# Kernel optimization log

Measured on AMD Instinct MI355X. Metric: run time of the kernel, lower is better.

Reference implementation:

```python
import jax, jax.numpy as jnp
import numpy as np
from jax import lax

TWN_THRESHOLD_FACTOR = 0.05
BN_EPS = 1e-5


@jax.custom_vjp
def _ternary_quant(w, t):
    return (w > t).astype(w.dtype) - (w < -t).astype(w.dtype)

def _tq_fwd(w, t):
    mask = (w > t) | (w < -t)
    return _ternary_quant(w, t), mask

def _tq_bwd(mask, g):
    return (g * mask.astype(g.dtype), jnp.zeros((), g.dtype))

_ternary_quant.defvjp(_tq_fwd, _tq_bwd)


def quantize(w):
    # threshold is detached in the original (weight.detach().abs().max())
    t = TWN_THRESHOLD_FACTOR * jnp.max(jnp.abs(lax.stop_gradient(w)))
    return _ternary_quant(w, t)


def conv2d(x, w, b):
    # x: [N,C,H,W], w: [O,I,K,K], valid conv, stride 1
    y = lax.conv_general_dilated(x, w, (1, 1), 'VALID',
                                 dimension_numbers=('NCHW', 'OIHW', 'NCHW'))
    return y + b[None, :, None, None]


def maxpool2(x):
    return lax.reduce_window(x, -jnp.inf, lax.max,
                             (1, 1, 2, 2), (1, 1, 2, 2), 'VALID')


def bn2d(x, g, b):
    # training-mode batch norm over (N,H,W), biased variance
    m = jnp.mean(x, (0, 2, 3), keepdims=True)
    v = jnp.mean(jnp.square(x - m), (0, 2, 3), keepdims=True)
    return (x - m) * lax.rsqrt(v + BN_EPS) * g[None, :, None, None] + b[None, :, None, None]


def bn1d(x, g, b):
    m = jnp.mean(x, 0, keepdims=True)
    v = jnp.mean(jnp.square(x - m), 0, keepdims=True)
    return (x - m) * lax.rsqrt(v + BN_EPS) * g[None, :] + b[None, :]


def setup_inputs() -> dict:
    key = jax.random.key(0)
    ks = jax.random.split(key, 12)
    N = 4096
    inp = {
        'x': jax.random.normal(ks[0], (N, 1, 28, 28), jnp.float32),
        'w1': jax.random.normal(ks[1], (32, 1, 5, 5), jnp.float32) * 0.2,
        'b1': jnp.zeros((32,), jnp.float32),
        'g1': jnp.ones((32,), jnp.float32),
        'be1': jnp.zeros((32,), jnp.float32),
        'w2': jax.random.normal(ks[2], (64, 32, 5, 5), jnp.float32) * 0.05,
        'b2': jnp.zeros((64,), jnp.float32),
        'g2': jnp.ones((64,), jnp.float32),
        'be2': jnp.zeros((64,), jnp.float32),
        'wf1': jax.random.normal(ks[3], (512, 1024), jnp.float32) * 0.03,
        'bf1': jnp.zeros((512,), jnp.float32),
        'g3': jnp.ones((512,), jnp.float32),
        'be3': jnp.zeros((512,), jnp.float32),
        'wf2': jax.random.normal(ks[4], (10, 512), jnp.float32) * 0.04,
        'bf2': jnp.zeros((10,), jnp.float32),
    }
    return inp


def reference(x, w1, b1, g1, be1, w2, b2, g2, be2, wf1, bf1, g3, be3, wf2, bf2):
    h = jax.nn.relu(bn2d(conv2d(x, quantize(w1), b1), g1, be1))     # [N,32,24,24]
    h = maxpool2(h)                                                  # [N,32,12,12]
    h = jax.nn.relu(bn2d(conv2d(h, quantize(w2), b2), g2, be2))     # [N,64,8,8]
    h = maxpool2(h)                                                  # [N,64,4,4]
    h = h.reshape(h.shape[0], -1)                                    # [N,1024]
    h = jax.nn.relu(bn1d(h @ quantize(wf1).T + bf1, g3, be3))       # [N,512]
    return h @ quantize(wf2).T + bf2                                 # [N,10]
```

## Files before the change

kernel.cpp:

```cpp
#include <hip/hip_runtime.h>

#define TID ((int)threadIdx.x)
typedef unsigned short u16;
typedef short short8 __attribute__((ext_vector_type(8)));
typedef float f32x4 __attribute__((ext_vector_type(4)));

__device__ __forceinline__ u16 f2b(float f) {
    unsigned int x = __float_as_uint(f);
    return (u16)((x + 0x7fffu + ((x >> 16) & 1u)) >> 16);
}
__device__ __forceinline__ float b2f(u16 u) {
    return __uint_as_float(((unsigned int)u) << 16);
}

static constexpr size_t OFF_QW1   = 0;
static constexpr size_t OFF_QWF2  = 3200;
static constexpr size_t OFF_TMAX  = 23680;
static constexpr size_t OFF_SUM1C = 23808;
static constexpr size_t OFF_SSQ1C = 24832;
static constexpr size_t OFF_SUM2  = 25856, OFF_SSQ2 = 26112;
static constexpr size_t OFF_SUM3  = 26368, OFF_SSQ3 = 28416;
static constexpr size_t STATS_BEG = 23680, STATS_END = 30464;
static constexpr size_t OFF_QW2C  = 30720;
static constexpr size_t OFF_QWF1C = 133120;
static constexpr size_t OFF_Y1P   = 1181696;
static constexpr size_t OFF_Y2C   = 38930432;
static constexpr size_t OFF_H2C   = 72484864;
static constexpr size_t OFF_Y3    = 80873472;

__global__ __launch_bounds__(256) void absmax_k(const float* w1, const float* w2,
                                                const float* wf1, const float* wf2,
                                                unsigned int* tmaxbits) {
    int bid = blockIdx.x;
    int b, lb, nb; const float* src; long n;
    if (bid < 1)        { b = 0; src = w1;  n = 800;    lb = bid;       nb = 1;   }
    else if (bid < 9)   { b = 1; src = w2;  n = 51200;  lb = bid - 1;   nb = 8;   }
    else if (bid < 265) { b = 2; src = wf1; n = 524288; lb = bid - 9;   nb = 256; }
    else                { b = 3; src = wf2; n = 5120;   lb = bid - 265; nb = 1;   }
    float m = 0.f;
    for (long i = (long)lb * 256 + TID; i < n; i += (long)nb * 256)
        m = fmaxf(m, fabsf(src[i]));
    __shared__ float red[256];
    red[TID] = m; __syncthreads();
    for (int s = 128; s > 0; s >>= 1) {
        if (TID < s) red[TID] = fmaxf(red[TID], red[TID + s]);
        __syncthreads();
    }
    if (TID == 0) atomicMax(&tmaxbits[b], __float_as_uint(red[0]));
}

__global__ __launch_bounds__(256) void quant_all_k(const float* w1, const float* w2,
                                                   const float* wf1, const float* wf2,
                                                   float* qw1, u16* qw2c, u16* qwf1c,
                                                   float* qwf2, const unsigned int* tmax) {
    int bid = blockIdx.x;
    if (bid < 4) {
        int i = bid * 256 + TID; if (i >= 800) return;
        float t = 0.05f * __uint_as_float(tmax[0]);
        float v = w1[i];
        qw1[i] = (v > t) ? 1.f : ((v < -t) ? -1.f : 0.f);
    } else if (bid < 204) {
        int i = (bid - 4) * 256 + TID;
        float t = 0.05f * __uint_as_float(tmax[1]);
        int ic = i & 31, oc = (i >> 5) & 63, sh = i >> 11;
        float v = w2[(oc * 32 + ic) * 25 + sh];
        qw2c[i] = f2b((v > t) ? 1.f : ((v < -t) ? -1.f : 0.f));
    } else if (bid < 2252) {
        int i = (bid - 204) * 256 + TID;
        float t = 0.05f * __uint_as_float(tmax[2]);
        float v = wf1[i];
        qwf1c[i] = f2b((v > t) ? 1.f : ((v < -t) ? -1.f : 0.f));
    } else {
        int i = (bid - 2252) * 256 + TID;
        float t = 0.05f * __uint_as_float(tmax[3]);
        float v = wf2[i];
        qwf2[i] = (v > t) ? 1.f : ((v < -t) ? -1.f : 0.f);
    }
}

__global__ __launch_bounds__(256) void conv1_fused_k(const float* __restrict__ x,
                                                     const float* __restrict__ qw1,
                                                     u16* __restrict__ y1p,
                                                     float* sum1c, float* ssq1c) {
    __shared__ float wl[800];
    __shared__ float red[4][64];
    for (int i = TID; i < 800; i += 256) wl[i] = qw1[i];
    __syncthreads();
    int p = blockIdx.x * 256 + TID;
    int cg = p & 15, half = (p >> 4) & 1;
    int pr = p >> 5;
    int py = pr % 12, n = pr / 12;
    int l = TID & 63, wv = TID >> 6;
    const float* xb = x + n * 784 + (2 * py) * 28 + half * 12;
    float patch[6][16];
    #pragma unroll
    for (int r = 0; r < 6; r++) {
        const float4* rp = reinterpret_cast<const float4*>(xb + r * 28);
        #pragma unroll
        for (int qq = 0; qq < 4; qq++) {
            float4 v = rp[qq];
            patch[r][qq * 4 + 0] = v.x; patch[r][qq * 4 + 1] = v.y;
            patch[r][qq * 4 + 2] = v.z; patch[r][qq * 4 + 3] = v.w;
        }
    }
    int c0 = cg * 2;
    float st[4];
    float pm[2][6];
    #pragma unroll
    for (int cc = 0; cc < 2; cc++) {
        const float* wr = &wl[(c0 + cc) * 25];
        float a0[12] = {}, a1[12] = {};
        #pragma unroll
        for (int ky = 0; ky < 5; ky++)
            #pragma unroll
            for (int kx = 0; kx < 5; kx++) {
                float w = wr[ky * 5 + kx];
                #pragma unroll
                for (int ox = 0; ox < 12; ox++) {
                    a0[ox] = fmaf(patch[ky][ox + kx], w, a0[ox]);
                    a1[ox] = fmaf(patch[ky + 1][ox + kx], w, a1[ox]);
                }
            }
        float s = 0.f, q = 0.f;
        #pragma unroll
        for (int ox = 0; ox < 12; ox++) {
            s += a0[ox] + a1[ox];
            q = fmaf(a0[ox], a0[ox], q); q = fmaf(a1[ox], a1[ox], q);
        }
        st[cc] = s; st[2 + cc] = q;
        #pragma unroll
        for (int j = 0; j < 6; j++)
            pm[cc][j] = fmaxf(fmaxf(a0[2 * j], a0[2 * j + 1]),
                              fmaxf(a1[2 * j], a1[2 * j + 1]));
    }
    u16* base = y1p + (size_t)n * 4608 + (py * 12 + half * 6) * 32 + c0;
    #pragma unroll
    for (int j = 0; j < 6; j++) {
        unsigned int u = (unsigned int)f2b(pm[0][j]) | ((unsigned int)f2b(pm[1][j]) << 16);
        *reinterpret_cast<unsigned int*>(base + j * 32) = u;
    }
    #pragma unroll
    for (int t = 0; t < 4; t++) {
        st[t] += __shfl_xor(st[t], 16);
        st[t] += __shfl_xor(st[t], 32);
    }
    if (l < 16) {
        #pragma unroll
        for (int t = 0; t < 4; t++) red[wv][l * 4 + t] = st[t];
    }
    __syncthreads();
    if (TID < 64) {
        float v = red[0][TID] + red[1][TID] + red[2][TID] + red[3][TID];
        int t = TID & 3, ch = (TID >> 2) * 2 + (t & 1);
        float* dst = (t < 2 ? sum1c : ssq1c) + (blockIdx.x & 7) * 32 + ch;
        atomicAdd(dst, v);
    }
}

__global__ __launch_bounds__(256) void conv2_k(const u16* __restrict__ y1p,
                                               const u16* __restrict__ qw2c,
                                               u16* __restrict__ y2c,
                                               const float* sum1c, const float* ssq1c,
                                               const float* g1, const float* be1,
                                               float* sum, float* ssq) {
    __shared__ float4 hsm4[1176];
    __shared__ float scs[32], shs[32];
    char* hsraw = (char*)hsm4;
    int n0 = blockIdx.x * 8;
    int l = TID & 63, wv = TID >> 6;
    int oc0 = wv * 16;
    int lm = l & 15, lr = (l >> 3) & 1, ox = l & 7, bq = l >> 4;
    if (TID < 32) {
        float s = 0.f, q = 0.f;
        #pragma unroll
        for (int r = 0; r < 8; r++) { s += sum1c[r * 32 + TID]; q += ssq1c[r * 32 + TID]; }
        float m = s * (1.f / 2359296.f);
        float v = q * (1.f / 2359296.f) - m * m;
        float sc = g1[TID] / sqrtf(v + 1e-5f);
        scs[TID] = sc; shs[TID] = be1[TID] - m * sc;
    }
    __syncthreads();
    float scR[8], shR[8];
    {
        int b = TID & 3;
        #pragma unroll
        for (int j = 0; j < 8; j++) { scR[j] = scs[b * 8 + j]; shR[j] = shs[b * 8 + j]; }
    }
    short8 bw[25];
    #pragma unroll
    for (int sh = 0; sh < 25; sh++)
        bw[sh] = *reinterpret_cast<const short8*>(qw2c + ((size_t)sh * 64 + oc0 + lm) * 32 + bq * 8);
    int xy[5];
    #pragma unroll
    for (int kx = 0; kx < 5; kx++) {
        int xx = ox + kx;
        xy[kx] = lr * 784 + xx * 64 + (((bq + (xx >> 1)) & 3) * 16);
    }
    float sacc = 0.f, s2acc = 0.f;
    {
        const uint4* src = reinterpret_cast<const uint4*>(y1p + (size_t)n0 * 4608);
        #pragma unroll
        for (int k = 0; k < 3; k++) {
            if (k < 2 || TID < 64) {
                int i = TID + k * 256;
                int pix = i >> 2, b = i & 3;
                int y = pix / 12, xx = pix - y * 12;
                union { uint4 v; u16 u[8]; } in, out;
                in.v = src[i];
                #pragma unroll
                for (int j = 0; j < 8; j++)
                    out.u[j] = f2b(fmaxf(fmaf(b2f(in.u[j]), scR[j], shR[j]), 0.f));
                *reinterpret_cast<uint4*>(hsraw + y * 784 + xx * 64 + (((b + (xx >> 1)) & 3) * 16)) = out.v;
            }
        }
    }
    #pragma unroll 1
    for (int s = 0; s < 8; s++) {
        __syncthreads();
        if (s < 7) {
            const uint4* src = reinterpret_cast<const uint4*>(y1p + (size_t)(n0 + s + 1) * 4608);
            char* dst = hsraw + ((s + 1) & 1) * 9408;
            #pragma unroll
            for (int k = 0; k < 3; k++) {
                if (k < 2 || TID < 64) {
                    int i = TID + k * 256;
                    int pix = i >> 2, b = i & 3;
                    int y = pix / 12, xx = pix - y * 12;
                    union { uint4 v; u16 u[8]; } in, out;
                    in.v = src[i];
                    #pragma unroll
                    for (int j = 0; j < 8; j++)
                        out.u[j] = f2b(fmaxf(fmaf(b2f(in.u[j]), scR[j], shR[j]), 0.f));
                    *reinterpret_cast<uint4*>(dst + y * 784 + xx * 64 + (((b + (xx >> 1)) & 3) * 16)) = out.v;
                }
            }
        }
        const char* hb = hsraw + (s & 1) * 9408;
        f32x4 acc[4] = {{0.f,0.f,0.f,0.f},{0.f,0.f,0.f,0.f},{0.f,0.f,0.f,0.f},{0.f,0.f,0.f,0.f}};
        #pragma unroll
        for (int R = 0; R <= 10; R++) {
            short8 a[5];
            #pragma unroll
            for (int kx = 0; kx < 5; kx++)
                a[kx] = *reinterpret_cast<const short8*>(hb + xy[kx] + R * 784);
            #pragma unroll
            for (int mt = 0; mt < 4; mt++) {
                int ky = R - 2 * mt;
                if (ky < 0 || ky > 4) continue;
                #pragma unroll
                for (int kx = 0; kx < 5; kx++)
                    acc[mt] = __builtin_amdgcn_mfma_f32_16x16x32_bf16(a[kx], bw[ky * 5 + kx], acc[mt], 0, 0, 0);
            }
        }
        int n = n0 + s;
        #pragma unroll
        for (int mt = 0; mt < 4; mt++) {
            float v0 = acc[mt][0], v1 = acc[mt][1], v2 = acc[mt][2], v3 = acc[mt][3];
            sacc += v0 + v1 + v2 + v3;
            s2acc += v0 * v0 + v1 * v1 + v2 * v2 + v3 * v3;
            ushort4 u = make_ushort4(f2b(v0), f2b(v1), f2b(v2), f2b(v3));
            *reinterpret_cast<ushort4*>(y2c + (size_t)n * 4096 + (oc0 + lm) * 64 + mt * 16 + bq * 4) = u;
        }
    }
    sacc  += __shfl_xor(sacc, 16);  sacc  += __shfl_xor(sacc, 32);
    s2acc += __shfl_xor(s2acc, 16); s2acc += __shfl_xor(s2acc, 32);
    if (l < 16) { atomicAdd(&sum[oc0 + l], sacc); atomicAdd(&ssq[oc0 + l], s2acc); }
}

__global__ __launch_bounds__(256) void pool2_k(const u16* __restrict__ y2c,
                                               const float* sum2, const float* ssq2,
                                               const float* g2, const float* be2,
                                               u16* __restrict__ h2c) {
    int i = blockIdx.x * 256 + TID;
    int px = i & 3, py = (i >> 2) & 3, oc = (i >> 4) & 63, n = i >> 10;
    float m = sum2[oc] * (1.f / 262144.f);
    float v = ssq2[oc] * (1.f / 262144.f) - m * m;
    float s = g2[oc] / sqrtf(v + 1e-5f);
    float t = be2[oc] - m * s;
    size_t base = (size_t)n * 4096 + oc * 64 + (2 * py) * 8 + 2 * px;
    float a = b2f(y2c[base])     * s + t;
    float b = b2f(y2c[base + 1]) * s + t;
    float c = b2f(y2c[base + 8]) * s + t;
    float d = b2f(y2c[base + 9]) * s + t;
    float mm = fmaxf(fmaxf(fmaxf(fmaxf(0.f, a), b), c), d);
    h2c[i] = f2b(mm);
}

__global__ __launch_bounds__(256) void fc1_k(const u16* __restrict__ h2c,
                                             const u16* __restrict__ qwf1c,
                                             float* __restrict__ y3T,
                                             float* sum3, float* ssq3) {
    __shared__ float4 Asm[576], Bsm[576];
    u16* AsU = (u16*)Asm; u16* BsU = (u16*)Bsm;
    int m0 = blockIdx.x * 64, j0 = blockIdx.y * 64;
    int l = TID & 63, wv = TID >> 6;
    int lm = l & 15, q = l >> 4;
    int r0 = TID >> 3, c0 = TID & 7;
    f32x4 acc[4] = {{0.f,0.f,0.f,0.f},{0.f,0.f,0.f,0.f},{0.f,0.f,0.f,0.f},{0.f,0.f,0.f,0.f}};
    #pragma unroll 1
    for (int kc = 0; kc < 16; kc++) {
        int kk = kc * 64;
        if (kc) __syncthreads();
        #pragma unroll
        for (int i = 0; i < 2; i++) {
            int r = i * 32 + r0;
            *reinterpret_cast<float4*>(AsU + r * 72 + c0 * 8) =
                *reinterpret_cast<const float4*>(h2c + (size_t)(m0 + r) * 1024 + kk + c0 * 8);
            *reinterpret_cast<float4*>(BsU + r * 72 + c0 * 8) =
                *reinterpret_cast<const float4*>(qwf1c + (size_t)(j0 + r) * 1024 + kk + c0 * 8);
        }
        __syncthreads();
        #pragma unroll
        for (int half = 0; half < 2; half++) {
            short8 b = *reinterpret_cast<const short8*>(BsU + (wv * 16 + lm) * 72 + half * 32 + q * 8);
            #pragma unroll
            for (int mt = 0; mt < 4; mt++) {
                short8 a = *reinterpret_cast<const short8*>(AsU + (mt * 16 + lm) * 72 + half * 32 + q * 8);
                acc[mt] = __builtin_amdgcn_mfma_f32_16x16x32_bf16(a, b, acc[mt], 0, 0, 0);
            }
        }
    }
    float s = 0.f, s2 = 0.f;
    #pragma unroll
    for (int mt = 0; mt < 4; mt++) {
        *reinterpret_cast<f32x4*>(y3T + (size_t)(j0 + wv * 16 + lm) * 4096 + m0 + mt * 16 + q * 4) = acc[mt];
        #pragma unroll
        for (int i = 0; i < 4; i++) { float v = acc[mt][i]; s += v; s2 = fmaf(v, v, s2); }
    }
    s  += __shfl_xor(s, 16);  s  += __shfl_xor(s, 32);
    s2 += __shfl_xor(s2, 16); s2 += __shfl_xor(s2, 32);
    if (l < 16) {
        atomicAdd(&sum3[j0 + wv * 16 + l], s);
        atomicAdd(&ssq3[j0 + wv * 16 + l], s2);
    }
}

__global__ __launch_bounds__(256) void fc2_k(const float* __restrict__ y3T,
                                             const float* sum3, const float* ssq3,
                                             const float* g3, const float* be3,
                                             const float* __restrict__ qwf2,
                                             const float* bf2, float* __restrict__ out) {
    __shared__ float wlds[5120];
    __shared__ float part[15][160];
    __shared__ float sc3s[512], sh3s[512];
    for (int i = TID; i < 5120; i += 256) wlds[i] = qwf2[i];
    for (int k = TID; k < 512; k += 256) {
        float m = sum3[k] * (1.f / 4096.f);
        float v = ssq3[k] * (1.f / 4096.f) - m * m;
        float s = g3[k] / sqrtf(v + 1e-5f);
        sc3s[k] = s; sh3s[k] = be3[k] - m * s;
    }
    __syncthreads();
    int nl = TID & 15, ks = TID >> 4;
    int n = blockIdx.x * 16 + nl;
    float acc[10] = {};
    for (int k = ks * 32; k < ks * 32 + 32; k++) {
        float v = fmaxf(y3T[(size_t)k * 4096 + n] * sc3s[k] + sh3s[k], 0.f);
        #pragma unroll
        for (int o = 0; o < 10; o++) acc[o] = fmaf(v, wlds[o * 512 + k], acc[o]);
    }
    if (ks > 0) {
        #pragma unroll
        for (int o = 0; o < 10; o++) part[ks - 1][o * 16 + nl] = acc[o];
    }
    __syncthreads();
    if (ks == 0) {
        #pragma unroll
        for (int o = 0; o < 10; o++) {
            float r = acc[o] + bf2[o];
            #pragma unroll
            for (int j = 0; j < 15; j++) r += part[j][o * 16 + nl];
            out[n * 10 + o] = r;
        }
    }
}

extern "C" void kernel_launch(void* const* d_in, const int* in_sizes, int n_in,
                              void* d_out, int out_size, void* d_ws, size_t ws_size,
                              hipStream_t stream) {
    char* wsb = (char*)d_ws;
    const float* x   = (const float*)d_in[0];
    const float* w1  = (const float*)d_in[1];
    const float* g1  = (const float*)d_in[3];
    const float* be1 = (const float*)d_in[4];
    const float* w2  = (const float*)d_in[5];
    const float* g2  = (const float*)d_in[7];
    const float* be2 = (const float*)d_in[8];
    const float* wf1 = (const float*)d_in[9];
    const float* g3  = (const float*)d_in[11];
    const float* be3 = (const float*)d_in[12];
    const float* wf2 = (const float*)d_in[13];
    const float* bf2 = (const float*)d_in[14];
    float* out = (float*)d_out;

    unsigned int* tmax = (unsigned int*)(wsb + OFF_TMAX);
    float* qw1   = (float*)(wsb + OFF_QW1);
    float* qwf2  = (float*)(wsb + OFF_QWF2);
    u16*   qw2c  = (u16*)(wsb + OFF_QW2C);
    u16*   qwf1c = (u16*)(wsb + OFF_QWF1C);
    u16*   y1p   = (u16*)(wsb + OFF_Y1P);
    u16*   y2c   = (u16*)(wsb + OFF_Y2C);
    u16*   h2c   = (u16*)(wsb + OFF_H2C);
    float* y3    = (float*)(wsb + OFF_Y3);

    float* sum1c = (float*)(wsb + OFF_SUM1C); float* ssq1c = (float*)(wsb + OFF_SSQ1C);
    float* sum2  = (float*)(wsb + OFF_SUM2);  float* ssq2  = (float*)(wsb + OFF_SSQ2);
    float* sum3  = (float*)(wsb + OFF_SUM3);  float* ssq3  = (float*)(wsb + OFF_SSQ3);

    hipMemsetAsync(wsb + STATS_BEG, 0, STATS_END - STATS_BEG, stream);

    absmax_k<<<266, 256, 0, stream>>>(w1, w2, wf1, wf2, tmax);
    quant_all_k<<<2272, 256, 0, stream>>>(w1, w2, wf1, wf2, qw1, qw2c, qwf1c, qwf2, tmax);

    conv1_fused_k<<<6144, 256, 0, stream>>>(x, qw1, y1p, sum1c, ssq1c);
    conv2_k<<<512, 256, 0, stream>>>(y1p, qw2c, y2c, sum1c, ssq1c, g1, be1, sum2, ssq2);
    pool2_k<<<16384, 256, 0, stream>>>(y2c, sum2, ssq2, g2, be2, h2c);
    fc1_k<<<dim3(64, 8), 256, 0, stream>>>(h2c, qwf1c, y3, sum3, ssq3);
    fc2_k<<<256, 256, 0, stream>>>(y3, sum3, ssq3, g3, be3, qwf2, bf2, out);
}
```

Baseline: 235.0 us.

## Enlarge fc1 GEMM tiles with register-prefetch pipelining and vectorize pool loads

The fc1 GEMM moves from 64x64 tiles to 128x128 tiles, with each wave computing a 64x64 sub-tile as 4x4 MFMAs. It uses a 32-wide K step and prefetches the next K slice into registers while the current one is computed, which raises operand reuse per LDS read and hides global load latency. pool2 now reads pairs of adjacent bf16 values as one 32-bit load. The trade-off is a smaller grid (128 blocks on a chip with many CUs), which lowers occupancy and parallelism, and higher register pressure from the 16 accumulators.

```diff
diff --git a/kernel.cpp b/kernel.cpp
--- a/kernel.cpp
+++ b/kernel.cpp
@@ -278,10 +278,10 @@
     float s = g2[oc] / sqrtf(v + 1e-5f);
     float t = be2[oc] - m * s;
     size_t base = (size_t)n * 4096 + oc * 64 + (2 * py) * 8 + 2 * px;
-    float a = b2f(y2c[base])     * s + t;
-    float b = b2f(y2c[base + 1]) * s + t;
-    float c = b2f(y2c[base + 8]) * s + t;
-    float d = b2f(y2c[base + 9]) * s + t;
+    unsigned int u0 = *reinterpret_cast<const unsigned int*>(y2c + base);
+    unsigned int u1 = *reinterpret_cast<const unsigned int*>(y2c + base + 8);
+    float a = b2f((u16)u0) * s + t, b = b2f((u16)(u0 >> 16)) * s + t;
+    float c = b2f((u16)u1) * s + t, d = b2f((u16)(u1 >> 16)) * s + t;
     float mm = fmaxf(fmaxf(fmaxf(fmaxf(0.f, a), b), c), d);
     h2c[i] = f2b(mm);
 }
@@ -290,48 +290,68 @@
                                              const u16* __restrict__ qwf1c,
                                              float* __restrict__ y3T,
                                              float* sum3, float* ssq3) {
-    __shared__ float4 Asm[576], Bsm[576];
-    u16* AsU = (u16*)Asm; u16* BsU = (u16*)Bsm;
-    int m0 = blockIdx.x * 64, j0 = blockIdx.y * 64;
+    __shared__ __align__(16) u16 AsU[128 * 40];
+    __shared__ __align__(16) u16 BsU[128 * 40];
+    int m0 = blockIdx.x * 128, j0 = blockIdx.y * 128;
     int l = TID & 63, wv = TID >> 6;
     int lm = l & 15, q = l >> 4;
-    int r0 = TID >> 3, c0 = TID & 7;
-    f32x4 acc[4] = {{0.f,0.f,0.f,0.f},{0.f,0.f,0.f,0.f},{0.f,0.f,0.f,0.f},{0.f,0.f,0.f,0.f}};
+    int mw = (wv & 1) * 64, jw = (wv >> 1) * 64;
+    f32x4 acc[4][4] = {};
+    float4 pa[2], pb[2];
+    #pragma unroll
+    for (int i = 0; i < 2; i++) {
+        int e = TID + i * 256, m = e >> 2, s = e & 3;
+        pa[i] = *reinterpret_cast<const float4*>(h2c + (size_t)(m0 + m) * 1024 + s * 8);
+        pb[i] = *reinterpret_cast<const float4*>(qwf1c + (size_t)(j0 + m) * 1024 + s * 8);
+    }
     #pragma unroll 1
-    for (int kc = 0; kc < 16; kc++) {
-        int kk = kc * 64;
+    for (int kc = 0; kc < 32; kc++) {
         if (kc) __syncthreads();
         #pragma unroll
         for (int i = 0; i < 2; i++) {
-            int r = i * 32 + r0;
-            *reinterpret_cast<float4*>(AsU + r * 72 + c0 * 8) =
-                *reinterpret_cast<const float4*>(h2c + (size_t)(m0 + r) * 1024 + kk + c0 * 8);
-            *reinterpret_cast<float4*>(BsU + r * 72 + c0 * 8) =
-                *reinterpret_cast<const float4*>(qwf1c + (size_t)(j0 + r) * 1024 + kk + c0 * 8);
+            int e = TID + i * 256, m = e >> 2, s = e & 3;
+            *reinterpret_cast<float4*>(AsU + m * 40 + s * 8) = pa[i];
+            *reinterpret_cast<float4*>(BsU + m * 40 + s * 8) = pb[i];
         }
         __syncthreads();
-        #pragma unroll
-        for (int half = 0; half < 2; half++) {
-            short8 b = *reinterpret_cast<const short8*>(BsU + (wv * 16 + lm) * 72 + half * 32 + q * 8);
-            #pragma unroll
-            for (int mt = 0; mt < 4; mt++) {
-                short8 a = *reinterpret_cast<const short8*>(AsU + (mt * 16 + lm) * 72 + half * 32 + q * 8);
-                acc[mt] = __builtin_amdgcn_mfma_f32_16x16x32_bf16(a, b, acc[mt], 0, 0, 0);
+        if (kc < 31) {
+            int kk = (kc + 1) * 32;
+            #pragma unroll
+            for (int i = 0; i < 2; i++) {
+                int e = TID + i * 256, m = e >> 2, s = e & 3;
+                pa[i] = *reinterpret_cast<const float4*>(h2c + (size_t)(m0 + m) * 1024 + kk + s * 8);
+                pb[i] = *reinterpret_cast<const float4*>(qwf1c + (size_t)(j0 + m) * 1024 + kk + s * 8);
             }
         }
-    }
-    float s = 0.f, s2 = 0.f;
-    #pragma unroll
-    for (int mt = 0; mt < 4; mt++) {
-        *reinterpret_cast<f32x4*>(y3T + (size_t)(j0 + wv * 16 + lm) * 4096 + m0 + mt * 16 + q * 4) = acc[mt];
-        #pragma unroll
-        for (int i = 0; i < 4; i++) { float v = acc[mt][i]; s += v; s2 = fmaf(v, v, s2); }
-    }
-    s  += __shfl_xor(s, 16);  s  += __shfl_xor(s, 32);
-    s2 += __shfl_xor(s2, 16); s2 += __shfl_xor(s2, 32);
-    if (l < 16) {
-        atomicAdd(&sum3[j0 + wv * 16 + l], s);
-        atomicAdd(&ssq3[j0 + wv * 16 + l], s2);
+        short8 a[4], b[4];
+        #pragma unroll
+        for (int mi = 0; mi < 4; mi++)
+            a[mi] = *reinterpret_cast<const short8*>(AsU + (mw + mi * 16 + lm) * 40 + q * 8);
+        #pragma unroll
+        for (int ji = 0; ji < 4; ji++)
+            b[ji] = *reinterpret_cast<const short8*>(BsU + (jw + ji * 16 + lm) * 40 + q * 8);
+        #pragma unroll
+        for (int mi = 0; mi < 4; mi++)
+            #pragma unroll
+            for (int ji = 0; ji < 4; ji++)
+                acc[mi][ji] = __builtin_amdgcn_mfma_f32_16x16x32_bf16(a[mi], b[ji], acc[mi][ji], 0, 0, 0);
+    }
+    #pragma unroll
+    for (int ji = 0; ji < 4; ji++) {
+        int j = j0 + jw + ji * 16 + lm;
+        float s = 0.f, s2 = 0.f;
+        #pragma unroll
+        for (int mi = 0; mi < 4; mi++) {
+            *reinterpret_cast<f32x4*>(y3T + (size_t)j * 4096 + m0 + mw + mi * 16 + q * 4) = acc[mi][ji];
+            #pragma unroll
+            for (int i = 0; i < 4; i++) { float v = acc[mi][ji][i]; s += v; s2 = fmaf(v, v, s2); }
+        }
+        s  += __shfl_xor(s, 16);  s  += __shfl_xor(s, 32);
+        s2 += __shfl_xor(s2, 16); s2 += __shfl_xor(s2, 32);
+        if (l < 16) {
+            atomicAdd(&sum3[j0 + jw + ji * 16 + l], s);
+            atomicAdd(&ssq3[j0 + jw + ji * 16 + l], s2);
+        }
     }
 }
 
@@ -415,6 +435,6 @@
     conv1_fused_k<<<6144, 256, 0, stream>>>(x, qw1, y1p, sum1c, ssq1c);
     conv2_k<<<512, 256, 0, stream>>>(y1p, qw2c, y2c, sum1c, ssq1c, g1, be1, sum2, ssq2);
     pool2_k<<<16384, 256, 0, stream>>>(y2c, sum2, ssq2, g2, be2, h2c);
-    fc1_k<<<dim3(64, 8), 256, 0, stream>>>(h2c, qwf1c, y3, sum3, ssq3);
+    fc1_k<<<dim3(32, 4), 256, 0, stream>>>(h2c, qwf1c, y3, sum3, ssq3);
     fc2_k<<<256, 256, 0, stream>>>(y3, sum3, ssq3, g3, be3, qwf2, bf2, out);
 }
```

Result: slower. 262.9 us (+11.9%).
